# Kernel tuning notes

Hardware: AMD Instinct MI355X
Metric: run time of the kernel (lower is better)

The kernel has to match this reference:

```python
import jax, jax.numpy as jnp
import numpy as np

D = 512          # feature dim
N = 4095         # context length
LMBD = 0.9       # eligibility-trace decay
DIM = 2 * D + 1  # 1025
CTX = N + 1      # 4096


def make_M(n: int, lmbd: float) -> jnp.ndarray:
    # M[row, col] = lmbd**(row-col) for col <= row < n, col < n; last row and
    # last column are all zero (M[-1, -1] explicitly zeroed in the original).
    i = jnp.arange(n, dtype=jnp.int32)
    diff = i[:, None] - i[None, :]
    core = jnp.where(diff >= 0, jnp.float32(lmbd) ** jnp.maximum(diff, 0).astype(jnp.float32), 0.0)
    M = jnp.zeros((n + 1, n + 1), dtype=jnp.float32)
    return M.at[:n, :n].set(core)


def setup_inputs() -> dict:
    key = jax.random.key(0)
    kz, kp, kq = jax.random.split(key, 3)
    Z = jax.random.normal(kz, (DIM, CTX), dtype=jnp.float32)
    # nn.Parameter(torch.empty(...)) is uninitialized in the source; use small
    # random values as stand-ins for trained parameters.
    P = jax.random.normal(kp, (DIM, DIM), dtype=jnp.float32) * 0.02
    Q = jax.random.normal(kq, (DIM, DIM), dtype=jnp.float32) * 0.02
    M = make_M(N, LMBD)
    return {"Z": Z, "P": P, "Q": Q, "M": M}


def reference(Z, P, Q, M):
    # X = Z^T Q Z : (CTX, CTX) bilinear attention scores
    X = jnp.einsum("dn,de,em->nm", Z, Q, Z)
    A = jax.nn.softmax(X, axis=-1)          # activation
    # Z + (1/n) * P @ Z @ M @ A ; contract left-to-right to keep (DIM, CTX) intermediates
    PZ = P @ Z                               # (DIM, CTX)
    PZM = PZ @ M                             # (DIM, CTX), M lower-tri decay
    return Z + (1.0 / N) * (PZM @ A)
```

## Files before the change

kernel.cpp:

```cpp
#include <hip/hip_runtime.h>


#define LMBD 0.9f
#define CTXN 4096
#define DIMN 1025
#define DP 1152
#define KE 1088

#define KSPLIT 1024
#define PSTRIDE ((size_t)DP * CTXN)

typedef __bf16 bf16x8 __attribute__((ext_vector_type(8)));
typedef float f32x4 __attribute__((ext_vector_type(4)));
typedef long lx2 __attribute__((ext_vector_type(2)));

__device__ __forceinline__ unsigned short f2bf(float f) {
  union { float f; unsigned u; } v; v.f = f;
  unsigned r = v.u + 0x7FFFu + ((v.u >> 16) & 1u);
  return (unsigned short)(r >> 16);
}
__device__ __forceinline__ float bf2f(unsigned short h) {
  union { unsigned u; float f; } v; v.u = ((unsigned)h) << 16;
  return v.f;
}

__device__ __forceinline__ void gld_lds16(const void* g, void* l) {
  __builtin_amdgcn_global_load_lds(
      (const __attribute__((address_space(1))) unsigned int*)g,
      (__attribute__((address_space(3))) unsigned int*)l, 16, 0, 0);
}

template <int MODE, int TM, int TN>
__device__ __forceinline__ void gemm_body(
    const unsigned short* __restrict__ A, const unsigned short* __restrict__ B,
    void* __restrict__ Cout, int K, int lda, int ldb, int ldc, int bi, int bj,
    float* __restrict__ pmax, float* __restrict__ psum) {
  constexpr int FI = TM / 32, FJ = TN / 32;
  __shared__ unsigned short sA[TM * 64];
  __shared__ unsigned short sB[TN * 64];
  const int tid = threadIdx.x;
  const int wave = tid >> 6;
  const int lane = tid & 63;
  const long i0 = (long)bi * TM;
  const long j0 = (long)bj * TN;
  const int wm = (wave & 1) * (TM / 2);
  const int wn = (wave >> 1) * (TN / 2);

  f32x4 acc[FI][FJ] = {};

  const int srow8 = lane >> 3;
  const int gk = ((lane & 7) - srow8) & 7;
  const int mrow = lane & 15;
  const int q2 = lane >> 4;

  for (int k0 = 0; k0 < K; k0 += 64) {
    __syncthreads();
#pragma unroll
    for (int c = 0; c < TM / 32; ++c) {
      const int q = wave * (TM / 32) + c;
      gld_lds16(A + (i0 + q * 8 + srow8) * (long)lda + k0 + gk * 8, &sA[q * 512]);
    }
#pragma unroll
    for (int c = 0; c < TN / 32; ++c) {
      const int q = wave * (TN / 32) + c;
      gld_lds16(B + (j0 + q * 8 + srow8) * (long)ldb + k0 + gk * 8, &sB[q * 512]);
    }
    __syncthreads();
#pragma unroll
    for (int kk = 0; kk < 2; ++kk) {
      const int slot = ((kk * 4 + q2) + mrow) & 7;
      bf16x8 af[FI], bfr[FJ];
#pragma unroll
      for (int i = 0; i < FI; ++i)
        af[i] = *(const bf16x8*)&sA[(wm + i * 16 + mrow) * 64 + slot * 8];
#pragma unroll
      for (int j = 0; j < FJ; ++j)
        bfr[j] = *(const bf16x8*)&sB[(wn + j * 16 + mrow) * 64 + slot * 8];
#pragma unroll
      for (int i = 0; i < FI; ++i)
#pragma unroll
        for (int j = 0; j < FJ; ++j)
          acc[i][j] =
              __builtin_amdgcn_mfma_f32_16x16x32_bf16(af[i], bfr[j], acc[i][j], 0, 0, 0);
    }
  }

  const int lr = (lane >> 4) * 4;
  const int lc = lane & 15;
#pragma unroll
  for (int i = 0; i < FI; ++i) {
#pragma unroll
    for (int j = 0; j < FJ; ++j) {
#pragma unroll
      for (int r = 0; r < 4; ++r) {
        const long row = i0 + wm + i * 16 + lr + r;
        const long col = j0 + wn + j * 16 + lc;
        const float v = acc[i][j][r];
        if (MODE == 1) ((float*)Cout)[row * ldc + col] = v;
        else ((unsigned short*)Cout)[row * ldc + col] = f2bf(v);
      }
    }
  }

  if constexpr (MODE == 4) {
    float* sMax = (float*)sA;
    float* sSum = (float*)sB;
    const int k8 = (wave & 1) * 4 + (lane >> 4);
    __syncthreads();
#pragma unroll
    for (int j = 0; j < FJ; ++j) {
      float m = -1e30f;
#pragma unroll
      for (int i = 0; i < FI; ++i)
#pragma unroll
        for (int r = 0; r < 4; ++r) m = fmaxf(m, acc[i][j][r]);
      float sv = 0.f;
#pragma unroll
      for (int i = 0; i < FI; ++i)
#pragma unroll
        for (int r = 0; r < 4; ++r) sv += __expf(acc[i][j][r] - m);
      const int c = wn + j * 16 + lc;
      sMax[c * 8 + k8] = m;
      sSum[c * 8 + k8] = sv;
    }
    __syncthreads();
    if (tid < 128) {
      float m = -1e30f;
#pragma unroll
      for (int k = 0; k < 8; ++k) m = fmaxf(m, sMax[tid * 8 + k]);
      float sv = 0.f;
#pragma unroll
      for (int k = 0; k < 8; ++k) sv += sSum[tid * 8 + k] * __expf(sMax[tid * 8 + k] - m);
      pmax[(size_t)bi * CTXN + j0 + tid] = m;
      psum[(size_t)bi * CTXN + j0 + tid] = sv;
    }
  }
}

__global__ __launch_bounds__(256, 2) void gemm_xt(
    const unsigned short* __restrict__ QZT, const unsigned short* __restrict__ ZbT,
    unsigned short* __restrict__ XT, float* __restrict__ pmax,
    float* __restrict__ psum) {
  gemm_body<4, 128, 128>(QZT, ZbT, XT, KE, DP, DP, CTXN, blockIdx.x, blockIdx.y, pmax,
                         psum);
}

__global__ __launch_bounds__(256, 2) void gemm_dual(
    const unsigned short* __restrict__ ZbT, const unsigned short* __restrict__ Qb,
    unsigned short* __restrict__ QZT, const unsigned short* __restrict__ Pb,
    float* __restrict__ PZ) {
  const unsigned g = blockIdx.x;
  if (g < 544) {
    gemm_body<0, 128, 64>(ZbT, Qb, QZT, KE, DP, DP, DP, g & 31, g >> 5, nullptr,
                          nullptr);
  } else {
    const unsigned h = g - 544;
    gemm_body<1, 64, 128>(Pb, ZbT, PZ, KE, DP, DP, CTXN, h >> 5, h & 31, nullptr,
                          nullptr);
  }
}

__global__ __launch_bounds__(256, 2) void gemm_fp8_splitk(
    const unsigned char* __restrict__ A, const unsigned char* __restrict__ B,
    unsigned short* __restrict__ Cout) {
  __shared__ unsigned char sA[128 * 64];
  __shared__ unsigned char sB[128 * 64];
  const int tid = threadIdx.x;
  const int wave = tid >> 6;
  const int lane = tid & 63;
  const unsigned g = blockIdx.x;
  const unsigned bj = g & 31;
  const unsigned t = g >> 5;
  const unsigned bi = t >> 2;
  const unsigned bz = t & 3;
  const long i0 = (long)bi * 128;
  const long j0 = (long)bj * 128;
  const int wm = (wave & 1) * 64;
  const int wn = (wave >> 1) * 64;
  const int kb = bz * KSPLIT;
  Cout += (size_t)bz * PSTRIDE;

  f32x4 acc[4][4] = {};
  const int srow = lane >> 2;
  const int skc = (((lane & 3) - (lane >> 3)) & 3) * 16;
  const int mrow = lane & 15;
  const int slot = ((((lane >> 4) + (mrow >> 1)) & 3)) * 16;

  for (int k0 = kb; k0 < kb + KSPLIT; k0 += 64) {
    __syncthreads();
#pragma unroll
    for (int c = 0; c < 2; ++c) {
      const int q = wave * 2 + c;
      gld_lds16(A + (i0 + q * 16 + srow) * (long)CTXN + k0 + skc, &sA[q * 1024]);
      gld_lds16(B + (j0 + q * 16 + srow) * (long)CTXN + k0 + skc, &sB[q * 1024]);
    }
    __syncthreads();
    lx2 af[4], bfr[4];
#pragma unroll
    for (int i = 0; i < 4; ++i)
      af[i] = *(const lx2*)&sA[(wm + i * 16 + mrow) * 64 + slot];
#pragma unroll
    for (int j = 0; j < 4; ++j)
      bfr[j] = *(const lx2*)&sB[(wn + j * 16 + mrow) * 64 + slot];
#pragma unroll
    for (int i = 0; i < 4; ++i)
#pragma unroll
      for (int j = 0; j < 4; ++j) {
        acc[i][j] = __builtin_amdgcn_mfma_f32_16x16x32_fp8_fp8(af[i].x, bfr[j].x,
                                                               acc[i][j], 0, 0, 0);
        acc[i][j] = __builtin_amdgcn_mfma_f32_16x16x32_fp8_fp8(af[i].y, bfr[j].y,
                                                               acc[i][j], 0, 0, 0);
      }
  }

  const int lr = (lane >> 4) * 4;
  const int lc = lane & 15;
#pragma unroll
  for (int i = 0; i < 4; ++i)
#pragma unroll
    for (int j = 0; j < 4; ++j)
#pragma unroll
      for (int r = 0; r < 4; ++r) {
        const long row = i0 + wm + i * 16 + lr + r;
        if (row < DIMN)
          Cout[row * (long)CTXN + j0 + wn + j * 16 + lc] = f2bf(acc[i][j][r]);
      }
}

__global__ void reduce_kernel(const unsigned short* __restrict__ Pt,
                              const float* __restrict__ Z, float* __restrict__ out) {
  const size_t idx = ((size_t)blockIdx.x * 256 + threadIdx.x) * 4;
  float ax = 0.f, ay = 0.f, az = 0.f, aw = 0.f;
#pragma unroll
  for (int z = 0; z < 4; ++z) {
    const ushort4 v = *(const ushort4*)&Pt[(size_t)z * PSTRIDE + idx];
    ax += bf2f(v.x); ay += bf2f(v.y); az += bf2f(v.z); aw += bf2f(v.w);
  }
  const f32x4 zv = *(const f32x4*)&Z[idx];
  f32x4 o;
  o[0] = zv[0] + ax * 0.00390625f;
  o[1] = zv[1] + ay * 0.00390625f;
  o[2] = zv[2] + az * 0.00390625f;
  o[3] = zv[3] + aw * 0.00390625f;
  *(f32x4*)&out[idx] = o;
}

__global__ void prep_kernel(const float* __restrict__ Z, const float* __restrict__ Q,
                            const float* __restrict__ P,
                            unsigned short* __restrict__ ZbT,
                            unsigned short* __restrict__ Qb,
                            unsigned short* __restrict__ Pb) {
  __shared__ float tile[32][33];
  const unsigned g = blockIdx.x;
  const int tid = threadIdx.x;
  if (g < 4352) {
    const int n0 = (g & 127) * 32, e0 = (g >> 7) * 32;
    const int tx = tid & 31, ty = tid >> 5;
#pragma unroll
    for (int k = 0; k < 4; ++k) {
      const int e = e0 + ty + k * 8;
      tile[ty + k * 8][tx] = (e < DIMN) ? Z[(size_t)e * CTXN + n0 + tx] : 0.f;
    }
    __syncthreads();
#pragma unroll
    for (int k = 0; k < 4; ++k) {
      const int n = n0 + ty + k * 8;
      ZbT[(size_t)n * DP + e0 + tx] = f2bf(tile[tx][ty + k * 8]);
    }
  } else {
    const unsigned id2 = g - 4352;
    const int mat = id2 >= 1296;
    const float* src = mat ? P : Q;
    unsigned short* dst = mat ? Pb : Qb;
    const unsigned e0 = (id2 - (mat ? 1296u : 0u)) * 1024u + tid * 4u;
    const unsigned r = e0 / 1152u;
    const unsigned c = e0 - r * 1152u;
    ushort4 o;
    o.x = (r < DIMN && c + 0 < DIMN) ? f2bf(src[(size_t)r * DIMN + c + 0]) : 0;
    o.y = (r < DIMN && c + 1 < DIMN) ? f2bf(src[(size_t)r * DIMN + c + 1]) : 0;
    o.z = (r < DIMN && c + 2 < DIMN) ? f2bf(src[(size_t)r * DIMN + c + 2]) : 0;
    o.w = (r < DIMN && c + 3 < DIMN) ? f2bf(src[(size_t)r * DIMN + c + 3]) : 0;
    *(ushort4*)&dst[(size_t)r * DP + c] = o;
  }
}

__global__ void red2_kernel(const float* __restrict__ pmax, const float* __restrict__ psum,
                            float* __restrict__ rowmax, float* __restrict__ inv_l) {
  const int n = blockIdx.x * 256 + threadIdx.x;
  float M = -1e30f;
  for (int c = 0; c < 32; ++c) M = fmaxf(M, pmax[(size_t)c * CTXN + n]);
  float s = 0.f;
  for (int c = 0; c < 32; ++c)
    s += psum[(size_t)c * CTXN + n] * __expf(pmax[(size_t)c * CTXN + n] - M);
  rowmax[n] = M;
  inv_l[n] = 1.0f / (4095.0f * s);
}

__global__ __launch_bounds__(256) void ewscan_kernel(
    const unsigned short* __restrict__ XT, const float* __restrict__ rowmax,
    unsigned int* __restrict__ ET, const float* __restrict__ PZ,
    const float* __restrict__ inv_l, unsigned char* __restrict__ PZMb) {
  __shared__ float sF[256];
  const unsigned g = blockIdx.x;
  const int t = threadIdx.x;
  if (g >= 1088) {
    const size_t idx = ((size_t)(g - 1088) * 256 + t) * 4;
    const ushort4 v = *(const ushort4*)&XT[idx];
    const int n = (int)(idx & 4095);
    const float4 rm = *(const float4*)&rowmax[n];
    unsigned p = __builtin_amdgcn_cvt_pk_fp8_f32(__expf(bf2f(v.x) - rm.x),
                                                 __expf(bf2f(v.y) - rm.y), 0, false);
    p = __builtin_amdgcn_cvt_pk_fp8_f32(__expf(bf2f(v.z) - rm.z),
                                        __expf(bf2f(v.w) - rm.w), p, true);
    ET[idx >> 2] = p;
    return;
  }
  const int d = g;
  const float* row = PZ + (size_t)d * CTXN;
  float x[16];
#pragma unroll
  for (int q = 0; q < 4; ++q) {
    const float4 v = *(const float4*)&row[t * 16 + q * 4];
    x[q * 4 + 0] = v.x; x[q * 4 + 1] = v.y; x[q * 4 + 2] = v.z; x[q * 4 + 3] = v.w;
  }
  if (t == 255) x[15] = 0.f;
  float loc[16];
  float run = 0.f;
#pragma unroll
  for (int i = 15; i >= 0; --i) { run = run * LMBD + x[i]; loc[i] = run; }
  float f = loc[0];
  sF[t] = f;
  __syncthreads();
  float mlt = 0.1853020188851841f;
  for (int step = 1; step < 256; step <<= 1) {
    const float other = (t + step < 256) ? sF[t + step] : 0.f;
    __syncthreads();
    f += mlt * other;
    mlt *= mlt;
    sF[t] = f;
    __syncthreads();
  }
  const float R = (t < 255) ? sF[t + 1] : 0.f;
  float il[16];
#pragma unroll
  for (int q = 0; q < 4; ++q) {
    const float4 v = *(const float4*)&inv_l[t * 16 + q * 4];
    il[q * 4 + 0] = v.x * 256.f; il[q * 4 + 1] = v.y * 256.f;
    il[q * 4 + 2] = v.z * 256.f; il[q * 4 + 3] = v.w * 256.f;
  }
  float o[16];
  float p = 1.f;
#pragma unroll
  for (int i = 15; i >= 0; --i) {
    p *= LMBD;
    o[i] = (loc[i] + p * R) * il[i];
  }
  unsigned w[4];
#pragma unroll
  for (int q = 0; q < 4; ++q) {
    unsigned pk = __builtin_amdgcn_cvt_pk_fp8_f32(o[q * 4 + 0], o[q * 4 + 1], 0, false);
    pk = __builtin_amdgcn_cvt_pk_fp8_f32(o[q * 4 + 2], o[q * 4 + 3], pk, true);
    w[q] = pk;
  }
  *(uint4*)&PZMb[(size_t)d * CTXN + t * 16] = make_uint4(w[0], w[1], w[2], w[3]);
}

extern "C" void kernel_launch(void* const* d_in, const int* in_sizes, int n_in,
                              void* d_out, int out_size, void* d_ws, size_t ws_size,
                              hipStream_t stream) {
  const float* Z = (const float*)d_in[0];
  const float* P = (const float*)d_in[1];
  const float* Q = (const float*)d_in[2];

  char* ws = (char*)d_ws;
  size_t off = 0;
  auto alloc = [&](size_t bytes) {
    void* p = ws + off;
    off += (bytes + 255) & ~(size_t)255;
    return p;
  };
  unsigned char* ET   = (unsigned char*)alloc((size_t)CTXN * CTXN);
  unsigned char* PZMb = (unsigned char*)alloc((size_t)DP * CTXN);
  float* rowmax       = (float*)alloc((size_t)CTXN * 4);
  float* inv_l        = (float*)alloc((size_t)CTXN * 4);
  char* pool = (char*)alloc(0);
  unsigned short* ZbT = (unsigned short*)alloc((size_t)CTXN * DP * 2);
  unsigned short* QZT = (unsigned short*)alloc((size_t)CTXN * DP * 2);
  unsigned short* XT  = (unsigned short*)alloc((size_t)CTXN * CTXN * 2);
  float* PZ           = (float*)alloc((size_t)DP * CTXN * 4);
  unsigned short* Qb  = (unsigned short*)alloc((size_t)DP * DP * 2);
  unsigned short* Pb  = (unsigned short*)alloc((size_t)DP * DP * 2);
  float* pmax         = (float*)alloc((size_t)32 * CTXN * 4);
  float* psum         = (float*)alloc((size_t)32 * CTXN * 4);
  unsigned short* partials = (unsigned short*)pool;
  if (off > ws_size) return;

  prep_kernel<<<6944, 256, 0, stream>>>(Z, Q, P, ZbT, Qb, Pb);

  gemm_dual<<<1088, 256, 0, stream>>>(ZbT, Qb, QZT, Pb, PZ);

  gemm_xt<<<dim3(32, 32), 256, 0, stream>>>(QZT, ZbT, XT, pmax, psum);

  red2_kernel<<<16, 256, 0, stream>>>(pmax, psum, rowmax, inv_l);

  ewscan_kernel<<<17472, 256, 0, stream>>>(XT, rowmax, (unsigned int*)ET, PZ, inv_l,
                                           PZMb);

  gemm_fp8_splitk<<<1152, 256, 0, stream>>>(PZMb, ET, partials);
  reduce_kernel<<<4100, 256, 0, stream>>>(partials, Z, (float*)d_out);
}
```

Baseline: 246.0 us.

## Replace X^T GEMM with 256x256-tile 8-wave pipelined kernel

Replaces the generic 128x128 GEMM used for the 4096x4096 score matrix with a dedicated 512-thread kernel computing 256x256 tiles as four 128x128 quadrants. Operand tiles are double-buffered in LDS through direct global-to-LDS loads, with explicit waitcnt, barrier and setprio scheduling so the next K-slab loads overlap the MFMAs. The fused column max and sum-exp partials now come from 16 row blocks, so the reduction kernel loops over 16 instead of 32. This aims to raise operand reuse and MFMA utilisation, at the cost of only 256 blocks (possible under-fill of the GPU) and heavy register use.

```diff
diff --git a/kernel.cpp b/kernel.cpp
--- a/kernel.cpp
+++ b/kernel.cpp
@@ -6,6 +6,7 @@
 #define DIMN 1025
 #define DP 1152
 #define KE 1088
+#define NT17 17
 
 #define KSPLIT 1024
 #define PSTRIDE ((size_t)DP * CTXN)
@@ -101,48 +102,160 @@
       }
     }
   }
-
-  if constexpr (MODE == 4) {
-    float* sMax = (float*)sA;
-    float* sSum = (float*)sB;
-    const int k8 = (wave & 1) * 4 + (lane >> 4);
-    __syncthreads();
-#pragma unroll
-    for (int j = 0; j < FJ; ++j) {
-      float m = -1e30f;
-#pragma unroll
-      for (int i = 0; i < FI; ++i)
-#pragma unroll
-        for (int r = 0; r < 4; ++r) m = fmaxf(m, acc[i][j][r]);
-      float sv = 0.f;
-#pragma unroll
-      for (int i = 0; i < FI; ++i)
-#pragma unroll
-        for (int r = 0; r < 4; ++r) sv += __expf(acc[i][j][r] - m);
-      const int c = wn + j * 16 + lc;
-      sMax[c * 8 + k8] = m;
-      sSum[c * 8 + k8] = sv;
-    }
-    __syncthreads();
-    if (tid < 128) {
-      float m = -1e30f;
-#pragma unroll
-      for (int k = 0; k < 8; ++k) m = fmaxf(m, sMax[tid * 8 + k]);
-      float sv = 0.f;
-#pragma unroll
-      for (int k = 0; k < 8; ++k) sv += sSum[tid * 8 + k] * __expf(sMax[tid * 8 + k] - m);
-      pmax[(size_t)bi * CTXN + j0 + tid] = m;
-      psum[(size_t)bi * CTXN + j0 + tid] = sv;
-    }
-  }
-}
-
-__global__ __launch_bounds__(256, 2) void gemm_xt(
+}
+
+#define LOADA8(bufi, qi)                                                      \
+  { _Pragma("unroll") for (int fi = 0; fi < 4; ++fi) {                        \
+      const int rowh = wr * 64 + fi * 16 + mrow;                              \
+      _Pragma("unroll") for (int kk = 0; kk < 2; ++kk) {                      \
+        const int slot = ((kk * 4 + q2) + mrow) & 7;                          \
+        af[fi][kk] = *(const bf16x8*)&sA[bufi][qi][rowh * 64 + slot * 8];     \
+      } } }
+#define LOADB8(bufi, qj)                                                      \
+  { _Pragma("unroll") for (int fj = 0; fj < 2; ++fj) {                        \
+      const int rowh = wc * 32 + fj * 16 + mrow;                              \
+      _Pragma("unroll") for (int kk = 0; kk < 2; ++kk) {                      \
+        const int slot = ((kk * 4 + q2) + mrow) & 7;                          \
+        bfr[fj][kk] = *(const bf16x8*)&sB[bufi][qj][rowh * 64 + slot * 8];    \
+      } } }
+#define STAGEA8(bufi, h, tt)                                                  \
+  { _Pragma("unroll") for (int c = 0; c < 2; ++c) {                           \
+      const int q = wave * 2 + c;                                             \
+      gld_lds16(Ab + (long)((h) * 128 + q * 8) * DP + (tt) * 64,              \
+                &sA[bufi][h][q * 512]); } }
+#define STAGEB8(bufi, h, tt)                                                  \
+  { _Pragma("unroll") for (int c = 0; c < 2; ++c) {                           \
+      const int q = wave * 2 + c;                                             \
+      gld_lds16(Bb + (long)((h) * 128 + q * 8) * DP + (tt) * 64,              \
+                &sB[bufi][h][q * 512]); } }
+#define MMAQ8(qi, qj)                                                         \
+  _Pragma("unroll") for (int kk = 0; kk < 2; ++kk)                            \
+  _Pragma("unroll") for (int fi = 0; fi < 4; ++fi)                            \
+  _Pragma("unroll") for (int fj = 0; fj < 2; ++fj)                            \
+      acc[qi][qj][fi][fj] = __builtin_amdgcn_mfma_f32_16x16x32_bf16(          \
+          af[fi][kk], bfr[fj][kk], acc[qi][qj][fi][fj], 0, 0, 0);
+#define PH_MID()                                                              \
+  __builtin_amdgcn_s_barrier();                                               \
+  asm volatile("s_waitcnt lgkmcnt(0)" ::: "memory");                          \
+  __builtin_amdgcn_sched_barrier(0);                                          \
+  __builtin_amdgcn_s_setprio(1)
+#define PH_END()                                                              \
+  __builtin_amdgcn_s_setprio(0);                                              \
+  __builtin_amdgcn_s_barrier()
+
+__global__ __launch_bounds__(512, 2) void gemm_xt8(
     const unsigned short* __restrict__ QZT, const unsigned short* __restrict__ ZbT,
     unsigned short* __restrict__ XT, float* __restrict__ pmax,
     float* __restrict__ psum) {
-  gemm_body<4, 128, 128>(QZT, ZbT, XT, KE, DP, DP, CTXN, blockIdx.x, blockIdx.y, pmax,
-                         psum);
+  __shared__ unsigned short sA[2][2][128 * 64];
+  __shared__ unsigned short sB[2][2][128 * 64];
+  const int tid = threadIdx.x;
+  const int wave = tid >> 6;
+  const int lane = tid & 63;
+  const int wr = wave >> 2;
+  const int wc = wave & 3;
+  const long i0 = (long)blockIdx.x * 256;
+  const long j0 = (long)blockIdx.y * 256;
+  const int srow8 = lane >> 3;
+  const int gk = ((lane & 7) - srow8) & 7;
+  const int mrow = lane & 15;
+  const int q2 = lane >> 4;
+
+  const unsigned short* Ab = QZT + (i0 + srow8) * (long)DP + gk * 8;
+  const unsigned short* Bb = ZbT + (j0 + srow8) * (long)DP + gk * 8;
+
+  f32x4 acc[2][2][4][2] = {};
+  bf16x8 af[4][2], bfr[2][2];
+
+  STAGEA8(0, 0, 0); STAGEB8(0, 0, 0); STAGEA8(0, 1, 0); STAGEB8(0, 1, 0);
+  STAGEB8(1, 0, 1); STAGEA8(1, 1, 1);
+  asm volatile("s_waitcnt vmcnt(4)" ::: "memory");
+  __builtin_amdgcn_s_barrier();
+
+#pragma unroll 1
+  for (int t = 0; t < NT17; ++t) {
+    const int buf = t & 1, nbuf = buf ^ 1;
+    LOADA8(buf, 0);
+    LOADB8(buf, 0);
+    if (t + 1 < NT17) STAGEA8(nbuf, 0, t + 1);
+    PH_MID();
+    MMAQ8(0, 0);
+    PH_END();
+    LOADA8(buf, 1);
+    if (t + 1 < NT17) STAGEB8(nbuf, 1, t + 1);
+    PH_MID();
+    MMAQ8(1, 0);
+    __builtin_amdgcn_s_setprio(0);
+    if (t < 16) asm volatile("s_waitcnt vmcnt(4)" ::: "memory");
+    else        asm volatile("s_waitcnt vmcnt(0)" ::: "memory");
+    __builtin_amdgcn_s_barrier();
+    LOADB8(buf, 1);
+    if (t + 2 < NT17) STAGEB8(buf, 0, t + 2);
+    PH_MID();
+    MMAQ8(1, 1);
+    PH_END();
+    LOADA8(buf, 0);
+    if (t + 2 < NT17) STAGEA8(buf, 1, t + 2);
+    PH_MID();
+    MMAQ8(0, 1);
+    __builtin_amdgcn_s_setprio(0);
+    if (t < 15)      asm volatile("s_waitcnt vmcnt(4)" ::: "memory");
+    else if (t == 15) asm volatile("s_waitcnt vmcnt(2)" ::: "memory");
+    __builtin_amdgcn_s_barrier();
+  }
+
+  const int lr = q2 * 4;
+#pragma unroll
+  for (int qi = 0; qi < 2; ++qi)
+#pragma unroll
+    for (int qj = 0; qj < 2; ++qj)
+#pragma unroll
+      for (int fi = 0; fi < 4; ++fi)
+#pragma unroll
+        for (int fj = 0; fj < 2; ++fj)
+#pragma unroll
+          for (int r = 0; r < 4; ++r) {
+            const long row = i0 + qi * 128 + wr * 64 + fi * 16 + lr + r;
+            const long col = j0 + qj * 128 + wc * 32 + fj * 16 + mrow;
+            XT[row * CTXN + col] = f2bf(acc[qi][qj][fi][fj][r]);
+          }
+
+  float* sMax = (float*)&sA[0][0][0];
+  float* sSum = (float*)&sB[0][0][0];
+  const int k8 = wr * 4 + q2;
+#pragma unroll
+  for (int qj = 0; qj < 2; ++qj)
+#pragma unroll
+    for (int fj = 0; fj < 2; ++fj) {
+      float m = -1e30f;
+#pragma unroll
+      for (int qi = 0; qi < 2; ++qi)
+#pragma unroll
+        for (int fi = 0; fi < 4; ++fi)
+#pragma unroll
+          for (int r = 0; r < 4; ++r) m = fmaxf(m, acc[qi][qj][fi][fj][r]);
+      float sv = 0.f;
+#pragma unroll
+      for (int qi = 0; qi < 2; ++qi)
+#pragma unroll
+        for (int fi = 0; fi < 4; ++fi)
+#pragma unroll
+          for (int r = 0; r < 4; ++r) sv += __expf(acc[qi][qj][fi][fj][r] - m);
+      const int c = qj * 128 + wc * 32 + fj * 16 + mrow;
+      sMax[c * 8 + k8] = m;
+      sSum[c * 8 + k8] = sv;
+    }
+  __syncthreads();
+  if (tid < 256) {
+    float m = -1e30f;
+#pragma unroll
+    for (int k = 0; k < 8; ++k) m = fmaxf(m, sMax[tid * 8 + k]);
+    float sv = 0.f;
+#pragma unroll
+    for (int k = 0; k < 8; ++k) sv += sSum[tid * 8 + k] * __expf(sMax[tid * 8 + k] - m);
+    pmax[(size_t)blockIdx.x * CTXN + j0 + tid] = m;
+    psum[(size_t)blockIdx.x * CTXN + j0 + tid] = sv;
+  }
 }
 
 __global__ __launch_bounds__(256, 2) void gemm_dual(
@@ -288,9 +401,9 @@
                             float* __restrict__ rowmax, float* __restrict__ inv_l) {
   const int n = blockIdx.x * 256 + threadIdx.x;
   float M = -1e30f;
-  for (int c = 0; c < 32; ++c) M = fmaxf(M, pmax[(size_t)c * CTXN + n]);
+  for (int c = 0; c < 16; ++c) M = fmaxf(M, pmax[(size_t)c * CTXN + n]);
   float s = 0.f;
-  for (int c = 0; c < 32; ++c)
+  for (int c = 0; c < 16; ++c)
     s += psum[(size_t)c * CTXN + n] * __expf(pmax[(size_t)c * CTXN + n] - M);
   rowmax[n] = M;
   inv_l[n] = 1.0f / (4095.0f * s);
@@ -399,7 +512,7 @@
 
   gemm_dual<<<1088, 256, 0, stream>>>(ZbT, Qb, QZT, Pb, PZ);
 
-  gemm_xt<<<dim3(32, 32), 256, 0, stream>>>(QZT, ZbT, XT, pmax, psum);
+  gemm_xt8<<<dim3(16, 16), 512, 0, stream>>>(QZT, ZbT, XT, pmax, psum);
 
   red2_kernel<<<16, 256, 0, stream>>>(pmax, psum, rowmax, inv_l);
 
```

Result: no change. 245.3 us (-0.3%).
